# Kernel tuning notes

Hardware: AMD Instinct MI355X
Metric: run time of the kernel (lower is better)

## Reference

```python
import jax, jax.numpy as jnp
import numpy as np

N = 16384      # number of points
DIM = 128      # feature dim
POS_DIM = 3
K = 16         # neighbors (init kwarg k)
SCALE = np.float32(np.sqrt(DIM))


def setup_inputs() -> dict:
    key = jax.random.key(0)
    ks = jax.random.split(key, 16)
    g = lambda i, shape: (jax.random.normal(ks[i], shape, dtype=jnp.float32) * 0.05)
    return {
        "x": jax.random.normal(ks[0], (N, DIM), dtype=jnp.float32),
        "pos": jax.random.uniform(ks[1], (N, POS_DIM), dtype=jnp.float32),
        # weights stored as (in, out); torch Linear applies x @ W.T + b
        "Wq": g(2, (DIM, DIM)),
        "Wk": g(3, (DIM, DIM)),
        "Wv": g(4, (DIM, DIM)),
        "mid_w1": g(5, (DIM, DIM)), "mid_b1": g(6, (DIM,)),
        "mid_w2": g(7, (DIM, DIM)), "mid_b2": g(8, (DIM,)),
        "pe_w1": g(9, (POS_DIM, DIM)), "pe_b1": g(10, (DIM,)),
        "pe_w2": g(11, (DIM, DIM)), "pe_b2": g(12, (DIM,)),
        "fin_w": g(13, (DIM, DIM)), "fin_b": g(14, (DIM,)),
    }


def _knn_indices(pos):
    # squared pairwise distances [N, N]; top-K smallest -> neighbor indices [N, K]
    sq = jnp.sum(pos * pos, axis=-1)
    d2 = sq[:, None] + sq[None, :] - 2.0 * (pos @ pos.T)
    _, ind = jax.lax.top_k(-d2, K)
    return ind


def reference(x, pos, Wq, Wk, Wv, mid_w1, mid_b1, mid_w2, mid_b2,
              pe_w1, pe_b1, pe_w2, pe_b2, fin_w, fin_b):
    ind = _knn_indices(pos)                    # [N, K] int32 (constant wrt grads)
    x_k = x[ind]                               # [N, K, D]
    pos_k = pos[ind]                           # [N, K, 3]
    rel = pos[:, None, :] - pos_k              # [N, K, 3]
    pe = jax.nn.relu(rel @ pe_w1 + pe_b1) @ pe_w2 + pe_b2    # [N, K, D]
    q = x @ Wq                                 # [N, D]
    h = q[:, None, :] - (x_k @ Wk) + pe        # [N, K, D]
    y = jax.nn.relu(h @ mid_w1 + mid_b1) @ mid_w2 + mid_b2   # [N, K, D]
    y = jax.nn.softmax(y / SCALE, axis=-2)     # softmax over neighbors K
    z = x_k @ Wv + pe                          # [N, K, D]
    agg = jnp.sum(y * z, axis=-2)              # [N, D]
    return agg @ fin_w + fin_b + x
```

## Files before the change

kernel.cpp:

```cpp
#include <hip/hip_runtime.h>
#include <hip/hip_bf16.h>

#define N_PTS 16384
#define DIMF  128
#define KNB   16
#define GRES  8
#define NCELL (GRES*GRES*GRES)

typedef __attribute__((ext_vector_type(8))) short bf16x8;
typedef __attribute__((ext_vector_type(4))) short bf16x4;
typedef __attribute__((ext_vector_type(4))) float f32x4;
typedef __attribute__((ext_vector_type(4))) unsigned int u32x4;
typedef __attribute__((ext_vector_type(2))) unsigned int u32x2;

__device__ __forceinline__ unsigned short f2b(float f){
  unsigned int u = __float_as_uint(f);
  u = u + 0x7fffu + ((u >> 16) & 1u);
  return (unsigned short)(u >> 16);
}
__device__ __forceinline__ unsigned cvtpk(float lo, float hi){
  unsigned r;
  asm("v_cvt_pk_bf16_f32 %0, %1, %2" : "=v"(r) : "v"(lo), "v"(hi));
  return r;
}
__device__ __forceinline__ float b2f(unsigned short u){
  return __uint_as_float(((unsigned)u) << 16);
}
__device__ __forceinline__ float b2fs(short s){
  return __uint_as_float(((unsigned)(unsigned short)s) << 16);
}
__device__ __forceinline__ float unsort_f(unsigned s){
  unsigned u = (s & 0x80000000u) ? (s ^ 0x80000000u) : ~s;
  return __uint_as_float(u);
}

__global__ __launch_bounds__(256) void count_kernel(const float* __restrict__ pos, int* __restrict__ cnt){
  int i = blockIdx.x*256 + threadIdx.x;
  float px = pos[i*3+0], py = pos[i*3+1], pz = pos[i*3+2];
  int cx = min(GRES-1, max(0,(int)(px*(float)GRES)));
  int cy = min(GRES-1, max(0,(int)(py*(float)GRES)));
  int cz = min(GRES-1, max(0,(int)(pz*(float)GRES)));
  atomicAdd(&cnt[(cz*GRES+cy)*GRES+cx], 1);
}

__global__ __launch_bounds__(256) void scan_kernel(const int* __restrict__ cnt, int* __restrict__ starts, int* __restrict__ fillp){
  __shared__ int wsum[4];
  int t = threadIdx.x;
  int lane = t & 63, w = t >> 6;
  int a = cnt[2*t], b = cnt[2*t+1];
  int s = a + b;
  int p = s;
  #pragma unroll
  for (int off = 1; off < 64; off <<= 1){
    int v = __shfl_up(p, off, 64);
    if (lane >= off) p += v;
  }
  if (lane == 63) wsum[w] = p;
  __syncthreads();
  int base = 0;
  for (int i = 0; i < w; ++i) base += wsum[i];
  int excl = base + p - s;
  starts[2*t]   = excl;     fillp[2*t]   = excl;
  starts[2*t+1] = excl + a; fillp[2*t+1] = excl + a;
}

__global__ __launch_bounds__(256) void scatter_pack(const float* __restrict__ pos, int* __restrict__ fillp,
                                                    float4* __restrict__ pos4, int* __restrict__ pidx,
                                                    int* __restrict__ inv,
                                                    const float* __restrict__ w0, const float* __restrict__ w1,
                                                    const float* __restrict__ w2, const float* __restrict__ w3,
                                                    const float* __restrict__ w4, const float* __restrict__ w5,
                                                    const float* __restrict__ w6,
                                                    short* __restrict__ dst){
  if (blockIdx.x < 64){
    int i = blockIdx.x*256 + threadIdx.x;
    float px = pos[i*3+0], py = pos[i*3+1], pz = pos[i*3+2];
    int cx = min(GRES-1, max(0,(int)(px*(float)GRES)));
    int cy = min(GRES-1, max(0,(int)(py*(float)GRES)));
    int cz = min(GRES-1, max(0,(int)(pz*(float)GRES)));
    int c = (cz*GRES+cy)*GRES+cx;
    float sq = __fadd_rn(__fadd_rn(__fmul_rn(px,px), __fmul_rn(py,py)), __fmul_rn(pz,pz));
    int s = atomicAdd(&fillp[c], 1);
    pos4[s] = make_float4(px, py, pz, sq);
    pidx[s] = i;
    inv[i] = s;
  } else {
    int pb = blockIdx.x - 64;
    int slot = pb >> 6;
    const float* src = (slot==0)?w0:(slot==1)?w1:(slot==2)?w2:(slot==3)?w3:(slot==4)?w4:(slot==5)?w5:w6;
    int f = (pb & 63)*256 + threadIdx.x;
    int j  = f & 7;
    int ln = (f >> 3) & 63;
    int ks = (f >> 9) & 3;
    int nt = f >> 11;
    int k = ks*32 + ((ln >> 4) << 3) + j;
    int n = nt*16 + (ln & 15);
    dst[slot*16384 + f] = (short)f2b(src[k*DIMF + n]);
  }
}

__global__ __launch_bounds__(256) void knn_query64(const float4* __restrict__ pos4, const int* __restrict__ pidx,
                                                   const int* __restrict__ starts, const int* __restrict__ cnt,
                                                   const int* __restrict__ inv,
                                                   int* __restrict__ ind_slot){
  __shared__ unsigned long long cand[4][64];
  int lane = threadIdx.x & 63;
  int wv   = threadIdx.x >> 6;
  int t = blockIdx.x*4 + wv;
  float4 qp = pos4[t];
  float qx = qp.x, qy = qp.y, qz = qp.z, qsq = qp.w;
  int cx = min(GRES-1, max(0,(int)(qx*(float)GRES)));
  int cy = min(GRES-1, max(0,(int)(qy*(float)GRES)));
  int cz = min(GRES-1, max(0,(int)(qz*(float)GRES)));
  int zlo = max(0,cz-1), zhi = min(GRES-1,cz+1);
  int ylo = max(0,cy-1), yhi = min(GRES-1,cy+1);
  int xlo = max(0,cx-1), xhi = min(GRES-1,cx+1);
  const double h = 0.125;
  double dqx=(double)qx, dqy=(double)qy, dqz=(double)qz;

  int nb = 0;
  if (lane < 27){
    int dz = lane/9 - 1, dy = (lane/3)%3 - 1, dx = lane%3 - 1;
    int zz = cz+dz, yy = cy+dy, xx = cx+dx;
    if (zz>=zlo && zz<=zhi && yy>=ylo && yy<=yhi && xx>=xlo && xx<=xhi)
      nb = cnt[(zz*GRES+yy)*GRES+xx];
  }
  #pragma unroll
  for (int o=1;o<64;o<<=1) nb += __shfl_xor(nb, o, 64);
  float V = (float)((zhi-zlo+1)*(yhi-ylo+1)*(xhi-xlo+1)) * 0.001953125f;
  float r3 = 3.8197186f * V / (float)nb;
  float tau2 = 2.0f * __powf(r3, 0.66666667f);

  int nfound = 0;
  bool okscan = false;
  for (int it = 0; it < 8; ++it){
    nfound = 0;
    for (int zz=zlo; zz<=zhi; ++zz)
    for (int yy=ylo; yy<=yhi; ++yy)
    for (int xx=xlo; xx<=xhi; ++xx){
      double mdx = fmax(0.0, fmax((double)xx*h - dqx, dqx - (double)(xx+1)*h));
      double mdy = fmax(0.0, fmax((double)yy*h - dqy, dqy - (double)(yy+1)*h));
      double mdz = fmax(0.0, fmax((double)zz*h - dqz, dqz - (double)(zz+1)*h));
      double md2 = mdx*mdx + mdy*mdy + mdz*mdz;
      if (md2 > (double)tau2 + 1.0e-5) continue;
      int c = (zz*GRES+yy)*GRES+xx;
      int s0 = starts[c], n = cnt[c];
      for (int b = 0; b < n; b += 64){
        int o = b + lane;
        bool valid = o < n;
        float d = 3.0e38f; int idx = 0;
        if (valid){
          float4 pc = pos4[s0+o];
          idx = pidx[s0+o];
          float dot = __fmaf_rn(qz, pc.z, __fmaf_rn(qy, pc.y, __fmul_rn(qx, pc.x)));
          d   = __fsub_rn(__fadd_rn(qsq, pc.w), __fmul_rn(2.0f, dot));
        }
        bool admit = valid && (d < tau2);
        unsigned long long mask = __ballot(admit);
        if (admit){
          int pos = nfound + (int)__popcll(mask & ((1ull<<lane)-1ull));
          if (pos < 64){
            unsigned su = __float_as_uint(d);
            su ^= (unsigned)((int)su >> 31) | 0x80000000u;
            cand[wv][pos] = ((unsigned long long)su << 32) | (unsigned)idx;
          }
        }
        nfound += (int)__popcll(mask);
      }
    }
    if (nfound > 64){ tau2 *= 0.7f; continue; }
    if (nfound < 16){ tau2 *= 2.0f; continue; }
    okscan = true; break;
  }

  bool needfb = !okscan;
  if (okscan){
    asm volatile("s_waitcnt lgkmcnt(0)" ::: "memory");
    __builtin_amdgcn_sched_barrier(0);
    unsigned long long key = (lane < nfound) ? cand[wv][lane] : ~0ull;

    #pragma unroll
    for (int k = 2; k <= 64; k <<= 1){
      #pragma unroll
      for (int j = k>>1; j >= 1; j >>= 1){
        unsigned long long other = __shfl_xor(key, j, 64);
        bool takeSmall = (((lane & k) == 0) != ((lane & j) != 0));
        bool less = other < key;
        key = (takeSmall == less) ? other : key;
      }
    }
    if (lane < 16) ind_slot[t*KNB + lane] = inv[(int)(unsigned)(key & 0xffffffffu)];

    unsigned long long k15 = __shfl(key, 15, 64);
    float b16 = unsort_f((unsigned)(k15 >> 32));
    double mg = 1.0e300;
    if (cx-1 > 0)      mg = fmin(mg, dqx - (double)(cx-1)*h);
    if (cx+1 < GRES-1) mg = fmin(mg, (double)(cx+2)*h - dqx);
    if (cy-1 > 0)      mg = fmin(mg, dqy - (double)(cy-1)*h);
    if (cy+1 < GRES-1) mg = fmin(mg, (double)(cy+2)*h - dqy);
    if (cz-1 > 0)      mg = fmin(mg, dqz - (double)(cz-1)*h);
    if (cz+1 < GRES-1) mg = fmin(mg, (double)(cz+2)*h - dqz);
    needfb = !(mg*mg > (double)b16 + 1.0e-5);
  }

  if (needfb){
    float bd[KNB]; int bi[KNB];
    #pragma unroll
    for (int k=0;k<KNB;++k){ bd[k] = 3.0e38f; bi[k] = 0x7fffffff; }
    for (int r = 0; r < GRES; ++r){
      int zl = max(0, cz-r), zh = min(GRES-1, cz+r);
      int yl = max(0, cy-r), yh = min(GRES-1, cy+r);
      int xl = max(0, cx-r), xh = min(GRES-1, cx+r);
      for (int zz = zl; zz <= zh; ++zz)
      for (int yy = yl; yy <= yh; ++yy)
      for (int xx = xl; xx <= xh; ++xx){
        int ring = max(abs(zz-cz), max(abs(yy-cy), abs(xx-cx)));
        if (ring != r) continue;
        int c = (zz*GRES+yy)*GRES+xx;
        int s0 = starts[c], e = s0 + cnt[c];
        for (int s = s0; s < e; ++s){
          float4 pc = pos4[s];
          int idx = pidx[s];
          float dot = __fmaf_rn(qz, pc.z, __fmaf_rn(qy, pc.y, __fmul_rn(qx, pc.x)));
          float d   = __fsub_rn(__fadd_rn(qsq, pc.w), __fmul_rn(2.0f, dot));
          bool adm = (d < bd[KNB-1]) || (d == bd[KNB-1] && idx < bi[KNB-1]);
          if (adm){
            #pragma unroll
            for (int p = KNB-1; p >= 1; --p){
              float pd = bd[p-1]; int pi = bi[p-1];
              bool sh  = (pd > d) || (pd == d && pi > idx);
              bool ins = (!sh) && ((bd[p] > d) || (bd[p] == d && bi[p] > idx));
              bd[p] = sh ? pd : (ins ? d   : bd[p]);
              bi[p] = sh ? pi : (ins ? idx : bi[p]);
            }
            bool s0b = (bd[0] > d) || (bd[0] == d && bi[0] > idx);
            if (s0b){ bd[0] = d; bi[0] = idx; }
          }
        }
      }
      if (bd[KNB-1] < 3.0e37f){
        double mg = 1.0e300;
        if (cx - r > 0)      mg = fmin(mg, dqx - (double)(cx-r)*h);
        if (cx + r < GRES-1) mg = fmin(mg, (double)(cx+r+1)*h - dqx);
        if (cy - r > 0)      mg = fmin(mg, dqy - (double)(cy-r)*h);
        if (cy + r < GRES-1) mg = fmin(mg, (double)(cy+r+1)*h - dqy);
        if (cz - r > 0)      mg = fmin(mg, dqz - (double)(cz-r)*h);
        if (cz + r < GRES-1) mg = fmin(mg, (double)(cz+r+1)*h - dqz);
        if (mg*mg > (double)bd[KNB-1] + 1.0e-5) break;
      }
    }
    if (lane < 16) ind_slot[t*KNB + lane] = inv[bi[lane]];
  }
}

__global__ __launch_bounds__(256) void proj_kernel(const float* __restrict__ x, const int* __restrict__ pidx,
                                                   const short* __restrict__ pw,
                                                   unsigned short* __restrict__ q, unsigned short* __restrict__ xk,
                                                   unsigned short* __restrict__ xv){
  __shared__ __align__(16) char Abuf[16384];
  int tid = threadIdx.x, lane = tid & 63, wv = tid >> 6;
  int r0 = blockIdx.x * 64;
  {
    int row = tid >> 2, q4 = tid & 3;
    int orig = pidx[r0 + row];
    const float4* xr = (const float4*)(x + (size_t)orig*DIMF + q4*32);
    #pragma unroll
    for (int i=0;i<4;++i){
      float4 a = xr[2*i], b = xr[2*i+1];
      u32x4 u;
      u[0] = cvtpk(a.x, a.y); u[1] = cvtpk(a.z, a.w);
      u[2] = cvtpk(b.x, b.y); u[3] = cvtpk(b.z, b.w);
      *(u32x4*)(&Abuf[row*256 + ((q4*64 + i*16) ^ ((row&7)<<4))]) = u;
    }
  }
  __syncthreads();
  #pragma unroll 1
  for (int w = 0; w < 3; ++w){
    const bf16x8* bw = (const bf16x8*)(pw + w*16384);
    unsigned short* dst = (w==0) ? q : (w==1) ? xk : xv;
    f32x4 acc[8];
    #pragma unroll
    for (int nt=0;nt<8;++nt) acc[nt] = (f32x4){0.f,0.f,0.f,0.f};
    #pragma unroll
    for (int ks=0;ks<4;++ks){
      int ra = wv*16 + (lane&15);
      int cb = ks*64 + ((lane>>4)<<4);
      bf16x8 a0 = *(const bf16x8*)(&Abuf[ra*256 + (cb ^ ((ra&7)<<4))]);
      #pragma unroll
      for (int nt=0;nt<8;++nt){
        bf16x8 b = bw[(nt*4+ks)*64 + lane];
        acc[nt] = __builtin_amdgcn_mfma_f32_16x16x32_bf16(a0, b, acc[nt], 0, 0, 0);
      }
    }
    #pragma unroll
    for (int nt=0;nt<8;++nt){
      int grow = r0 + wv*16 + ((lane>>4)<<2);
      int col = nt*16 + (lane&15);
      unsigned pk01 = cvtpk(acc[nt][0], acc[nt][1]);
      unsigned pk23 = cvtpk(acc[nt][2], acc[nt][3]);
      dst[(size_t)(grow+0)*DIMF + col] = (unsigned short)pk01;
      dst[(size_t)(grow+1)*DIMF + col] = (unsigned short)(pk01 >> 16);
      dst[(size_t)(grow+2)*DIMF + col] = (unsigned short)pk23;
      dst[(size_t)(grow+3)*DIMF + col] = (unsigned short)(pk23 >> 16);
    }
  }
}

__global__ __launch_bounds__(512, 2) void main_kernel(
    const float* __restrict__ x, const float4* __restrict__ pos4, const int* __restrict__ pidx,
    const float* __restrict__ pe_w1, const float* __restrict__ pe_b1, const float* __restrict__ pe_b2,
    const float* __restrict__ mid_b1, const float* __restrict__ mid_b2, const float* __restrict__ fin_b,
    const unsigned short* __restrict__ qarr, const unsigned short* __restrict__ xkarr,
    const unsigned short* __restrict__ xvarr,
    const int* __restrict__ ind_slot, const short* __restrict__ pw,
    float* __restrict__ out)
{
  __shared__ __align__(16) char peLDS[32768];
  __shared__ __align__(16) char wbuf[32768];
  __shared__ float aggT[DIMF][9];
  __shared__ int indbuf[128];
  __shared__ int origbuf[8];
  int tid = threadIdx.x;
  int lane = tid & 63;
  int wv = tid >> 6;
  int t0 = blockIdx.x * 8;

  int g = lane >> 4, kl = lane & 15;
  int mt = wv;

  #define STAGE_W(slot) { \
    const char* gsrc = (const char*)(pw + (size_t)(slot)*16384) + wv*4096 + lane*16; \
    char* ldst = &wbuf[wv*4096]; \
    __builtin_amdgcn_global_load_lds(gsrc,        ldst,        16, 0, 0); \
    __builtin_amdgcn_global_load_lds(gsrc + 1024, ldst + 1024, 16, 0, 0); \
    __builtin_amdgcn_global_load_lds(gsrc + 2048, ldst + 2048, 16, 0, 0); \
    __builtin_amdgcn_global_load_lds(gsrc + 3072, ldst + 3072, 16, 0, 0); }

  if (tid < 128) indbuf[tid] = ind_slot[blockIdx.x*128 + tid];
  if (tid < 8) origbuf[tid] = pidx[t0 + tid];
  STAGE_W(3);
  __syncthreads();

  int nb4[4];
  #pragma unroll
  for (int r=0;r<4;++r) nb4[r] = indbuf[mt*16 + g*4 + r];
  int nbr = indbuf[mt*16 + kl];
  unsigned short zraw[8][4];
  #pragma unroll
  for (int nt=0;nt<8;++nt)
    #pragma unroll
    for (int r=0;r<4;++r)
      zraw[nt][r] = xvarr[(size_t)nb4[r]*DIMF + nt*16 + kl];

  bf16x8 tfrag[4];
  {
    float4 pq = pos4[t0+mt];
    float4 pn = pos4[nbr];
    float rx = pq.x-pn.x, ry = pq.y-pn.y, rz = pq.z-pn.z;
    #pragma unroll
    for (int ks=0;ks<4;++ks){
      int c0 = ks*32 + g*8;
      const float4* w0 = (const float4*)(pe_w1 + c0);
      const float4* w1 = (const float4*)(pe_w1 + DIMF + c0);
      const float4* w2 = (const float4*)(pe_w1 + 2*DIMF + c0);
      const float4* bb = (const float4*)(pe_b1 + c0);
      float4 wa0=w0[0], wa1=w0[1], wb0=w1[0], wb1=w1[1], wc0=w2[0], wc1=w2[1], wd0=bb[0], wd1=bb[1];
      float wa[8]={wa0.x,wa0.y,wa0.z,wa0.w,wa1.x,wa1.y,wa1.z,wa1.w};
      float wb[8]={wb0.x,wb0.y,wb0.z,wb0.w,wb1.x,wb1.y,wb1.z,wb1.w};
      float wc[8]={wc0.x,wc0.y,wc0.z,wc0.w,wc1.x,wc1.y,wc1.z,wc1.w};
      float wd[8]={wd0.x,wd0.y,wd0.z,wd0.w,wd1.x,wd1.y,wd1.z,wd1.w};
      float tv[8];
      #pragma unroll
      for (int j=0;j<8;++j)
        tv[j] = fmaxf(fmaf(rx, wa[j], fmaf(ry, wb[j], fmaf(rz, wc[j], wd[j]))), 0.f);
      u32x4 u;
      u[0] = cvtpk(tv[0], tv[1]); u[1] = cvtpk(tv[2], tv[3]);
      u[2] = cvtpk(tv[4], tv[5]); u[3] = cvtpk(tv[6], tv[7]);
      tfrag[ks] = __builtin_bit_cast(bf16x8, u);
    }
  }

  f32x4 acc[8];
  const bf16x8* bw = (const bf16x8*)wbuf;

  {
    #pragma unroll
    for (int nt=0;nt<8;++nt){
      float bv = pe_b2[nt*16 + kl];
      acc[nt] = (f32x4){bv,bv,bv,bv};
    }
    #pragma unroll
    for (int ks=0;ks<4;++ks){
      #pragma unroll
      for (int nt=0;nt<8;++nt){
        bf16x8 b = bw[(nt*4+ks)*64 + lane];
        acc[nt] = __builtin_amdgcn_mfma_f32_16x16x32_bf16(tfrag[ks], b, acc[nt], 0, 0, 0);
      }
    }
  }

  bf16x4 zb[8];
  int r0w = mt*16 + g*4;
  #pragma unroll
  for (int nt=0;nt<8;++nt){
    int col = nt*16 + kl;
    float p0 = acc[nt][0], p1 = acc[nt][1], p2 = acc[nt][2], p3 = acc[nt][3];
    unsigned pk01 = cvtpk(p0, p1), pk23 = cvtpk(p2, p3);
    *(unsigned short*)&peLDS[(r0w+0)*256 + ((col*2) ^ (((r0w+0)&7)<<4))] = (unsigned short)pk01;
    *(unsigned short*)&peLDS[(r0w+1)*256 + ((col*2) ^ (((r0w+1)&7)<<4))] = (unsigned short)(pk01 >> 16);
    *(unsigned short*)&peLDS[(r0w+2)*256 + ((col*2) ^ (((r0w+2)&7)<<4))] = (unsigned short)pk23;
    *(unsigned short*)&peLDS[(r0w+3)*256 + ((col*2) ^ (((r0w+3)&7)<<4))] = (unsigned short)(pk23 >> 16);
    float z0 = b2f(zraw[nt][0]) + p0;
    float z1 = b2f(zraw[nt][1]) + p1;
    float z2 = b2f(zraw[nt][2]) + p2;
    float z3 = b2f(zraw[nt][3]) + p3;
    u32x2 zu; zu[0] = cvtpk(z0, z1); zu[1] = cvtpk(z2, z3);
    zb[nt] = __builtin_bit_cast(bf16x4, zu);
  }

  bf16x8 q8[4], k8[4];
  {
    const unsigned short* qrow = qarr + (size_t)(t0+mt)*DIMF;
    const unsigned short* krow = xkarr + (size_t)nbr*DIMF;
    #pragma unroll
    for (int ks=0;ks<4;++ks){
      int c0 = ks*32 + g*8;
      q8[ks] = *(const bf16x8*)(qrow + c0);
      k8[ks] = *(const bf16x8*)(krow + c0);
    }
  }
  __syncthreads();
  STAGE_W(4);

  bf16x8 hfrag[4];
  {
    int row = mt*16 + kl;
    #pragma unroll
    for (int ks=0;ks<4;++ks){
      int c0 = ks*32 + g*8;
      bf16x8 p8 = *(const bf16x8*)(&peLDS[row*256 + ((c0*2) ^ ((row&7)<<4))]);
      float hf[8];
      #pragma unroll
      for (int j=0;j<8;++j)
        hf[j] = (b2fs(q8[ks][j]) - b2fs(k8[ks][j])) + b2fs(p8[j]);
      u32x4 u;
      u[0] = cvtpk(hf[0], hf[1]); u[1] = cvtpk(hf[2], hf[3]);
      u[2] = cvtpk(hf[4], hf[5]); u[3] = cvtpk(hf[6], hf[7]);
      hfrag[ks] = __builtin_bit_cast(bf16x8, u);
    }
  }
  __syncthreads();

  {
    #pragma unroll
    for (int nt=0;nt<8;++nt){
      float bv = mid_b1[nt*16 + kl];
      acc[nt] = (f32x4){bv,bv,bv,bv};
    }
    #pragma unroll
    for (int ks=0;ks<4;++ks){
      #pragma unroll
      for (int nt=0;nt<8;++nt){
        bf16x8 b = bw[(nt*4+ks)*64 + lane];
        acc[nt] = __builtin_amdgcn_mfma_f32_16x16x32_bf16(hfrag[ks], b, acc[nt], 0, 0, 0);
      }
    }
  }
  __syncthreads();
  STAGE_W(5);
  #pragma unroll
  for (int nt=0;nt<8;++nt){
    int col = nt*16 + kl;
    unsigned pk01 = cvtpk(fmaxf(acc[nt][0],0.f), fmaxf(acc[nt][1],0.f));
    unsigned pk23 = cvtpk(fmaxf(acc[nt][2],0.f), fmaxf(acc[nt][3],0.f));
    *(unsigned short*)&peLDS[(r0w+0)*256 + ((col*2) ^ (((r0w+0)&7)<<4))] = (unsigned short)pk01;
    *(unsigned short*)&peLDS[(r0w+1)*256 + ((col*2) ^ (((r0w+1)&7)<<4))] = (unsigned short)(pk01 >> 16);
    *(unsigned short*)&peLDS[(r0w+2)*256 + ((col*2) ^ (((r0w+2)&7)<<4))] = (unsigned short)pk23;
    *(unsigned short*)&peLDS[(r0w+3)*256 + ((col*2) ^ (((r0w+3)&7)<<4))] = (unsigned short)(pk23 >> 16);
  }
  __syncthreads();

  {
    #pragma unroll
    for (int nt=0;nt<8;++nt){
      float bv = mid_b2[nt*16 + kl];
      acc[nt] = (f32x4){bv,bv,bv,bv};
    }
    #pragma unroll
    for (int ks=0;ks<4;++ks){
      int ra = mt*16 + kl;
      int cb = ks*64 + g*16;
      bf16x8 a0 = *(const bf16x8*)(&peLDS[ra*256 + (cb ^ ((ra&7)<<4))]);
      #pragma unroll
      for (int nt=0;nt<8;++nt){
        bf16x8 b = bw[(nt*4+ks)*64 + lane];
        acc[nt] = __builtin_amdgcn_mfma_f32_16x16x32_bf16(a0, b, acc[nt], 0, 0, 0);
      }
    }
  }
  __syncthreads();
  STAGE_W(6);

  {
    const float invS = 0.08838834764831843f;
    #pragma unroll
    for (int nt=0;nt<8;++nt){
      f32x4 y = acc[nt];
      float mx = fmaxf(fmaxf(y[0],y[1]), fmaxf(y[2],y[3]));
      mx = fmaxf(mx, __shfl_xor(mx, 16, 64));
      mx = fmaxf(mx, __shfl_xor(mx, 32, 64));
      float e0 = __expf((y[0]-mx)*invS);
      float e1 = __expf((y[1]-mx)*invS);
      float e2 = __expf((y[2]-mx)*invS);
      float e3 = __expf((y[3]-mx)*invS);
      float ssum = e0+e1+e2+e3;
      ssum += __shfl_xor(ssum, 16, 64);
      ssum += __shfl_xor(ssum, 32, 64);
      bf16x4 zv = zb[nt];
      float ps = (e0*b2fs(zv[0]) + e1*b2fs(zv[1]) + e2*b2fs(zv[2]) + e3*b2fs(zv[3])) / ssum;
      ps += __shfl_xor(ps, 16, 64);
      ps += __shfl_xor(ps, 32, 64);
      if (lane < 16) aggT[nt*16 + lane][mt] = ps;
    }
  }
  __syncthreads();

  {
    f32x4 facc = (f32x4){0.f,0.f,0.f,0.f};
    #pragma unroll
    for (int ks=0;ks<4;++ks){
      int c0 = ks*32 + g*8;
      float av[8];
      #pragma unroll
      for (int j=0;j<8;++j)
        av[j] = (kl < 8) ? aggT[c0+j][kl] : 0.f;
      u32x4 u;
      u[0] = cvtpk(av[0], av[1]); u[1] = cvtpk(av[2], av[3]);
      u[2] = cvtpk(av[4], av[5]); u[3] = cvtpk(av[6], av[7]);
      bf16x8 a = __builtin_bit_cast(bf16x8, u);
      bf16x8 b = bw[(wv*4+ks)*64 + lane];
      facc = __builtin_amdgcn_mfma_f32_16x16x32_bf16(a, b, facc, 0, 0, 0);
    }
    int col = wv*16 + kl;
    float fb = fin_b[col];
    if (g < 2){
      #pragma unroll
      for (int r=0;r<4;++r){
        int prow = g*4 + r;
        int o = origbuf[prow];
        out[(size_t)o*DIMF + col] = facc[r] + fb + x[(size_t)o*DIMF + col];
      }
    }
  }
  #undef STAGE_W
}

extern "C" void kernel_launch(void* const* d_in, const int* in_sizes, int n_in,
                              void* d_out, int out_size, void* d_ws, size_t ws_size,
                              hipStream_t stream)
{
  (void)in_sizes; (void)n_in; (void)out_size; (void)ws_size;
  const float* x      = (const float*)d_in[0];
  const float* pos    = (const float*)d_in[1];
  const float* Wq     = (const float*)d_in[2];
  const float* Wk     = (const float*)d_in[3];
  const float* Wv     = (const float*)d_in[4];
  const float* mid_w1 = (const float*)d_in[5];
  const float* mid_b1 = (const float*)d_in[6];
  const float* mid_w2 = (const float*)d_in[7];
  const float* mid_b2 = (const float*)d_in[8];
  const float* pe_w1  = (const float*)d_in[9];
  const float* pe_b1  = (const float*)d_in[10];
  const float* pe_w2  = (const float*)d_in[11];
  const float* pe_b2  = (const float*)d_in[12];
  const float* fin_w  = (const float*)d_in[13];
  const float* fin_b  = (const float*)d_in[14];
  float* out = (float*)d_out;
  char* ws = (char*)d_ws;

  int*    cellcnt = (int*)   (ws + 0);
  int*    fillp   = (int*)   (ws + 4096);
  int*    starts  = (int*)   (ws + 8192);
  int*    pidx    = (int*)   (ws + 49152);
  float4* pos4    = (float4*)(ws + 114688);
  int*    ind     = (int*)   (ws + 376832);
  short*  pw      = (short*) (ws + 1425408);
  int*    inv     = (int*)   (ws + 1654784);
  unsigned short* qarr  = (unsigned short*)(ws + 1720320);
  unsigned short* xkarr = (unsigned short*)(ws + 5914624);
  unsigned short* xvarr = (unsigned short*)(ws + 10108928);

  hipMemsetAsync(cellcnt, 0, NCELL*sizeof(int), stream);
  count_kernel  <<<N_PTS/256, 256, 0, stream>>>(pos, cellcnt);
  scan_kernel   <<<1,         256, 0, stream>>>(cellcnt, starts, fillp);
  scatter_pack  <<<64 + 7*64, 256, 0, stream>>>(pos, fillp, pos4, pidx, inv,
                                                Wq, Wk, Wv, pe_w2, mid_w1, mid_w2, fin_w, pw);
  knn_query64   <<<N_PTS/4,   256, 0, stream>>>(pos4, pidx, starts, cellcnt, inv, ind);
  proj_kernel   <<<N_PTS/64,  256, 0, stream>>>(x, pidx, pw, qarr, xkarr, xvarr);
  main_kernel   <<<N_PTS/8,   512, 0, stream>>>(x, pos4, pidx, pe_w1, pe_b1, pe_b2, mid_b1, mid_b2, fin_b,
                                                qarr, xkarr, xvarr, ind, pw, out);
}
```

Measured before the change: 163.6 us.

## Halve weight LDS buffer, stage weights in halves, raise occupancy to four blocks

The weight staging buffer shrinks from 32KB to 16KB, and each 128x128 weight matrix is now loaded into LDS in two halves with a barrier between them. The launch bound goes from 2 to 4 blocks per CU, and the aggregate scratch is stored as bf16. The final projection reads its weights straight from global memory instead of LDS. The aim is higher occupancy through a smaller LDS footprint, at the cost of more barriers, serialized half-matrix loads, and tighter register limits that could cause spills.

```diff
diff --git a/kernel.cpp b/kernel.cpp
--- a/kernel.cpp
+++ b/kernel.cpp
@@ -306,7 +306,7 @@
   }
 }
 
-__global__ __launch_bounds__(512, 2) void main_kernel(
+__global__ __launch_bounds__(512, 4) void main_kernel(
     const float* __restrict__ x, const float4* __restrict__ pos4, const int* __restrict__ pidx,
     const float* __restrict__ pe_w1, const float* __restrict__ pe_b1, const float* __restrict__ pe_b2,
     const float* __restrict__ mid_b1, const float* __restrict__ mid_b2, const float* __restrict__ fin_b,
@@ -316,8 +316,8 @@
     float* __restrict__ out)
 {
   __shared__ __align__(16) char peLDS[32768];
-  __shared__ __align__(16) char wbuf[32768];
-  __shared__ float aggT[DIMF][9];
+  __shared__ __align__(16) char wbuf[16384];
+  __shared__ unsigned short aggTb[DIMF][9];
   __shared__ int indbuf[128];
   __shared__ int origbuf[8];
   int tid = threadIdx.x;
@@ -328,17 +328,18 @@
   int g = lane >> 4, kl = lane & 15;
   int mt = wv;
 
-  #define STAGE_W(slot) { \
-    const char* gsrc = (const char*)(pw + (size_t)(slot)*16384) + wv*4096 + lane*16; \
-    char* ldst = &wbuf[wv*4096]; \
+  #define STAGE_H(slot, half) { \
+    const char* gsrc = (const char*)(pw + (size_t)(slot)*16384) + (half)*16384 + wv*2048 + lane*16; \
+    char* ldst = &wbuf[wv*2048]; \
     __builtin_amdgcn_global_load_lds(gsrc,        ldst,        16, 0, 0); \
-    __builtin_amdgcn_global_load_lds(gsrc + 1024, ldst + 1024, 16, 0, 0); \
-    __builtin_amdgcn_global_load_lds(gsrc + 2048, ldst + 2048, 16, 0, 0); \
-    __builtin_amdgcn_global_load_lds(gsrc + 3072, ldst + 3072, 16, 0, 0); }
+    __builtin_amdgcn_global_load_lds(gsrc + 1024, ldst + 1024, 16, 0, 0); }
+
+  const bf16x8* bwh = (const bf16x8*)wbuf;
+  f32x4 acc[8];
 
   if (tid < 128) indbuf[tid] = ind_slot[blockIdx.x*128 + tid];
   if (tid < 8) origbuf[tid] = pidx[t0 + tid];
-  STAGE_W(3);
+  STAGE_H(3, 0);
   __syncthreads();
 
   int nb4[4];
@@ -380,24 +381,37 @@
     }
   }
 
-  f32x4 acc[8];
-  const bf16x8* bw = (const bf16x8*)wbuf;
-
+  #pragma unroll
+  for (int nt=0;nt<8;++nt){
+    float bv = pe_b2[nt*16 + kl];
+    acc[nt] = (f32x4){bv,bv,bv,bv};
+  }
+  #pragma unroll
+  for (int ks=0;ks<4;++ks)
+    #pragma unroll
+    for (int nt=0;nt<4;++nt)
+      acc[nt] = __builtin_amdgcn_mfma_f32_16x16x32_bf16(tfrag[ks], bwh[(nt*4+ks)*64 + lane], acc[nt], 0, 0, 0);
+  __syncthreads();
+  STAGE_H(3, 1);
+  bf16x8 q8[4], k8[4];
   {
-    #pragma unroll
-    for (int nt=0;nt<8;++nt){
-      float bv = pe_b2[nt*16 + kl];
-      acc[nt] = (f32x4){bv,bv,bv,bv};
-    }
+    const unsigned short* qrow = qarr + (size_t)(t0+mt)*DIMF;
+    const unsigned short* krow = xkarr + (size_t)nbr*DIMF;
     #pragma unroll
     for (int ks=0;ks<4;++ks){
-      #pragma unroll
-      for (int nt=0;nt<8;++nt){
-        bf16x8 b = bw[(nt*4+ks)*64 + lane];
-        acc[nt] = __builtin_amdgcn_mfma_f32_16x16x32_bf16(tfrag[ks], b, acc[nt], 0, 0, 0);
-      }
-    }
-  }
+      int c0 = ks*32 + g*8;
+      q8[ks] = *(const bf16x8*)(qrow + c0);
+      k8[ks] = *(const bf16x8*)(krow + c0);
+    }
+  }
+  __syncthreads();
+  #pragma unroll
+  for (int ks=0;ks<4;++ks)
+    #pragma unroll
+    for (int nt=4;nt<8;++nt)
+      acc[nt] = __builtin_amdgcn_mfma_f32_16x16x32_bf16(tfrag[ks], bwh[((nt&3)*4+ks)*64 + lane], acc[nt], 0, 0, 0);
+  __syncthreads();
+  STAGE_H(4, 0);
 
   bf16x4 zb[8];
   int r0w = mt*16 + g*4;
@@ -417,20 +431,7 @@
     u32x2 zu; zu[0] = cvtpk(z0, z1); zu[1] = cvtpk(z2, z3);
     zb[nt] = __builtin_bit_cast(bf16x4, zu);
   }
-
-  bf16x8 q8[4], k8[4];
-  {
-    const unsigned short* qrow = qarr + (size_t)(t0+mt)*DIMF;
-    const unsigned short* krow = xkarr + (size_t)nbr*DIMF;
-    #pragma unroll
-    for (int ks=0;ks<4;++ks){
-      int c0 = ks*32 + g*8;
-      q8[ks] = *(const bf16x8*)(qrow + c0);
-      k8[ks] = *(const bf16x8*)(krow + c0);
-    }
-  }
-  __syncthreads();
-  STAGE_W(4);
+  __syncthreads();
 
   bf16x8 hfrag[4];
   {
@@ -449,25 +450,27 @@
       hfrag[ks] = __builtin_bit_cast(bf16x8, u);
     }
   }
-  __syncthreads();
-
-  {
-    #pragma unroll
-    for (int nt=0;nt<8;++nt){
-      float bv = mid_b1[nt*16 + kl];
-      acc[nt] = (f32x4){bv,bv,bv,bv};
-    }
-    #pragma unroll
-    for (int ks=0;ks<4;++ks){
-      #pragma unroll
-      for (int nt=0;nt<8;++nt){
-        bf16x8 b = bw[(nt*4+ks)*64 + lane];
-        acc[nt] = __builtin_amdgcn_mfma_f32_16x16x32_bf16(hfrag[ks], b, acc[nt], 0, 0, 0);
-      }
-    }
-  }
-  __syncthreads();
-  STAGE_W(5);
+
+  #pragma unroll
+  for (int nt=0;nt<8;++nt){
+    float bv = mid_b1[nt*16 + kl];
+    acc[nt] = (f32x4){bv,bv,bv,bv};
+  }
+  #pragma unroll
+  for (int ks=0;ks<4;++ks)
+    #pragma unroll
+    for (int nt=0;nt<4;++nt)
+      acc[nt] = __builtin_amdgcn_mfma_f32_16x16x32_bf16(hfrag[ks], bwh[(nt*4+ks)*64 + lane], acc[nt], 0, 0, 0);
+  __syncthreads();
+  STAGE_H(4, 1);
+  __syncthreads();
+  #pragma unroll
+  for (int ks=0;ks<4;++ks)
+    #pragma unroll
+    for (int nt=4;nt<8;++nt)
+      acc[nt] = __builtin_amdgcn_mfma_f32_16x16x32_bf16(hfrag[ks], bwh[((nt&3)*4+ks)*64 + lane], acc[nt], 0, 0, 0);
+  __syncthreads();
+  STAGE_H(5, 0);
   #pragma unroll
   for (int nt=0;nt<8;++nt){
     int col = nt*16 + kl;
@@ -480,26 +483,33 @@
   }
   __syncthreads();
 
+  bf16x8 ua[4];
   {
-    #pragma unroll
-    for (int nt=0;nt<8;++nt){
-      float bv = mid_b2[nt*16 + kl];
-      acc[nt] = (f32x4){bv,bv,bv,bv};
-    }
+    int ra = mt*16 + kl;
     #pragma unroll
     for (int ks=0;ks<4;++ks){
-      int ra = mt*16 + kl;
       int cb = ks*64 + g*16;
-      bf16x8 a0 = *(const bf16x8*)(&peLDS[ra*256 + (cb ^ ((ra&7)<<4))]);
-      #pragma unroll
-      for (int nt=0;nt<8;++nt){
-        bf16x8 b = bw[(nt*4+ks)*64 + lane];
-        acc[nt] = __builtin_amdgcn_mfma_f32_16x16x32_bf16(a0, b, acc[nt], 0, 0, 0);
-      }
-    }
-  }
-  __syncthreads();
-  STAGE_W(6);
+      ua[ks] = *(const bf16x8*)(&peLDS[ra*256 + (cb ^ ((ra&7)<<4))]);
+    }
+  }
+  #pragma unroll
+  for (int nt=0;nt<8;++nt){
+    float bv = mid_b2[nt*16 + kl];
+    acc[nt] = (f32x4){bv,bv,bv,bv};
+  }
+  #pragma unroll
+  for (int ks=0;ks<4;++ks)
+    #pragma unroll
+    for (int nt=0;nt<4;++nt)
+      acc[nt] = __builtin_amdgcn_mfma_f32_16x16x32_bf16(ua[ks], bwh[(nt*4+ks)*64 + lane], acc[nt], 0, 0, 0);
+  __syncthreads();
+  STAGE_H(5, 1);
+  __syncthreads();
+  #pragma unroll
+  for (int ks=0;ks<4;++ks)
+    #pragma unroll
+    for (int nt=4;nt<8;++nt)
+      acc[nt] = __builtin_amdgcn_mfma_f32_16x16x32_bf16(ua[ks], bwh[((nt&3)*4+ks)*64 + lane], acc[nt], 0, 0, 0);
 
   {
     const float invS = 0.08838834764831843f;
@@ -520,25 +530,22 @@
       float ps = (e0*b2fs(zv[0]) + e1*b2fs(zv[1]) + e2*b2fs(zv[2]) + e3*b2fs(zv[3])) / ssum;
       ps += __shfl_xor(ps, 16, 64);
       ps += __shfl_xor(ps, 32, 64);
-      if (lane < 16) aggT[nt*16 + lane][mt] = ps;
+      if (lane < 16) aggTb[nt*16 + lane][mt] = f2b(ps);
     }
   }
   __syncthreads();
 
   {
+    const bf16x8* bwf = (const bf16x8*)(pw + (size_t)6*16384);
     f32x4 facc = (f32x4){0.f,0.f,0.f,0.f};
     #pragma unroll
     for (int ks=0;ks<4;++ks){
       int c0 = ks*32 + g*8;
-      float av[8];
+      bf16x8 a;
       #pragma unroll
       for (int j=0;j<8;++j)
-        av[j] = (kl < 8) ? aggT[c0+j][kl] : 0.f;
-      u32x4 u;
-      u[0] = cvtpk(av[0], av[1]); u[1] = cvtpk(av[2], av[3]);
-      u[2] = cvtpk(av[4], av[5]); u[3] = cvtpk(av[6], av[7]);
-      bf16x8 a = __builtin_bit_cast(bf16x8, u);
-      bf16x8 b = bw[(wv*4+ks)*64 + lane];
+        a[j] = (kl < 8) ? (short)aggTb[c0+j][kl] : (short)0;
+      bf16x8 b = bwf[(wv*4+ks)*64 + lane];
       facc = __builtin_amdgcn_mfma_f32_16x16x32_bf16(a, b, facc, 0, 0, 0);
     }
     int col = wv*16 + kl;
@@ -552,7 +559,7 @@
       }
     }
   }
-  #undef STAGE_W
+  #undef STAGE_H
 }
 
 extern "C" void kernel_launch(void* const* d_in, const int* in_sizes, int n_in,
```

New measurement: 173.9 us. 1.06x slower.
